# Kernel tuning notes

Hardware: AMD Instinct MI355X
Metric: run time of the kernel (lower is better)

The kernel has to match this reference:

```python
import jax, jax.numpy as jnp
import numpy as np

DIM = 1024
HEADS = 16
DIM_HEAD = 64
INNER = HEADS * DIM_HEAD  # 1024
MAX_POS = 512
B, N = 2, 1024


def setup_inputs() -> dict:
    key = jax.random.key(0)
    ks = jax.random.split(key, 6)
    s = DIM ** -0.5
    x = jax.random.normal(ks[0], (B, N, DIM), dtype=jnp.float32)
    Wq = jax.random.normal(ks[1], (DIM, INNER), dtype=jnp.float32) * s
    Wkv = jax.random.normal(ks[2], (DIM, 2 * INNER), dtype=jnp.float32) * s
    Wo = jax.random.normal(ks[3], (INNER, DIM), dtype=jnp.float32) * (INNER ** -0.5)
    bo = jnp.zeros((DIM,), dtype=jnp.float32)
    rel_emb = jax.random.normal(ks[4], (2 * MAX_POS + 1, DIM_HEAD), dtype=jnp.float32)
    return {"x": x, "Wq": Wq, "Wkv": Wkv, "Wo": Wo, "bo": bo, "rel_emb": rel_emb}


def reference(x, Wq, Wkv, Wo, bo, rel_emb):
    b, n, _ = x.shape
    scale = DIM_HEAD ** -0.5
    q = x @ Wq                    # [b, n, inner]
    kv = x @ Wkv                  # [b, n, 2*inner]
    k, v = jnp.split(kv, 2, axis=-1)

    def split_heads(t):
        return t.reshape(b, n, HEADS, DIM_HEAD).transpose(0, 2, 1, 3)  # [b,h,n,d]

    q, k, v = map(split_heads, (q, k, v))
    dots = jnp.einsum('bhid,bhjd->bhij', q, k) * scale

    seq = jnp.arange(n)
    dist = jnp.clip(seq[:, None] - seq[None, :], -MAX_POS, MAX_POS) + MAX_POS  # [n, n]
    rel = rel_emb[dist]           # [n, n, d]
    pos_attn = jnp.einsum('bhnd,nrd->bhnr', q, rel) * scale
    dots = dots + pos_attn

    attn = jax.nn.softmax(dots, axis=-1)
    out = jnp.einsum('bhij,bhjd->bhid', attn, v)
    out = out.transpose(0, 2, 1, 3).reshape(b, n, INNER)
    return out @ Wo + bo
```

## Files before the change

### kernel.cpp

```cpp
#include <hip/hip_runtime.h>

typedef __bf16 bf16x8 __attribute__((ext_vector_type(8)));
typedef float f32x4 __attribute__((ext_vector_type(4)));

#define DEV __device__ __forceinline__

DEV unsigned short f2bf(float f) {
  union { float f; unsigned u; } x; x.f = f;
  unsigned r = x.u + 0x7FFFu + ((x.u >> 16) & 1u);
  return (unsigned short)(r >> 16);
}
DEV float bf2f(unsigned short h) {
  union { unsigned u; float f; } x; x.u = ((unsigned)h) << 16;
  return x.f;
}
DEV unsigned short bfc(float f) {
  union { __bf16 b; unsigned short u; } c; c.b = (__bf16)f; return c.u;
}

typedef __attribute__((address_space(3))) void* lds_vp;
typedef const __attribute__((address_space(1))) void* gbl_vp;
DEV void load_lds16(const unsigned short* gp, void* lp) {
  __builtin_amdgcn_global_load_lds((gbl_vp)(const void*)gp, (lds_vp)lp, 16, 0, 0);
}

__global__ __launch_bounds__(256)
void prep_k(const float* __restrict__ x, const float* __restrict__ rel,
            const float* __restrict__ bo, const float* __restrict__ Wq,
            const float* __restrict__ Wkv, const float* __restrict__ Wo,
            unsigned short* __restrict__ xb, unsigned short* __restrict__ relb,
            unsigned short* __restrict__ bob, unsigned short* __restrict__ WqkvT,
            unsigned short* __restrict__ WoT) {
  __shared__ unsigned short tile[32][33];
  const int bid = blockIdx.x, tid = threadIdx.x;
  if (bid < 2114) {
    const float* src; unsigned short* dst; long base; long n;
    if (bid < 2048)      { src = x;   dst = xb;   base = (long)bid * 1024;          n = 2097152; }
    else if (bid < 2113) { src = rel; dst = relb; base = (long)(bid - 2048) * 1024; n = 65600; }
    else                 { src = bo;  dst = bob;  base = 0;                          n = 1024; }
    long i = base + tid * 4;
    if (i < n) {
      float4 v = *(const float4*)&src[i];
      unsigned long long u = (unsigned long long)f2bf(v.x)
                           | ((unsigned long long)f2bf(v.y) << 16)
                           | ((unsigned long long)f2bf(v.z) << 32)
                           | ((unsigned long long)f2bf(v.w) << 48);
      *(unsigned long long*)&dst[i] = u;
    }
  } else {
    int id = bid - 2114;
    const float* src; unsigned short* dst; const int R = 1024; int C, txt, tyt;
    if (id < 1024)      { src = Wq;  dst = WqkvT;           C = 1024; txt = id & 31; tyt = id >> 5; }
    else if (id < 3072) { int l = id - 1024; src = Wkv; dst = WqkvT + 1048576; C = 2048; txt = l & 63; tyt = l >> 6; }
    else                { int l = id - 3072; src = Wo;  dst = WoT;             C = 1024; txt = l & 31; tyt = l >> 5; }
    int c0 = txt * 32, r0 = tyt * 32;
    int tx = tid & 31, ty = tid >> 5;
    #pragma unroll
    for (int i = 0; i < 4; ++i)
      tile[ty + i * 8][tx] = f2bf(src[(size_t)(r0 + ty + i * 8) * C + c0 + tx]);
    __syncthreads();
    #pragma unroll
    for (int i = 0; i < 4; ++i)
      dst[(size_t)(c0 + ty + i * 8) * R + r0 + tx] = tile[tx][ty + i * 8];
  }
}

DEV void stage16(const unsigned short* gbase, size_t gstride,
                 unsigned short* lbase, int r0, int lane) {
  #pragma unroll
  for (int t = 0; t < 2; ++t) {
    int r = r0 + t * 8 + (lane >> 3);
    int lc = (lane & 7) ^ (r & 7);
    load_lds16(&gbase[(size_t)r * gstride + lc * 8], &lbase[(size_t)(r0 + t * 8) * 64]);
  }
}
DEV bf16x8 read_swz(const unsigned short* buf, int row, int lc) {
  int pc = lc ^ (row & 7);
  return *(const bf16x8*)&buf[row * 64 + pc * 8];
}

__global__ __launch_bounds__(256)
void gemm_qkv(const unsigned short* __restrict__ A,
              const unsigned short* __restrict__ Bt,
              unsigned short* __restrict__ o0,
              unsigned short* __restrict__ o1,
              unsigned short* __restrict__ o2) {
  __shared__ __align__(16) unsigned short As[64 * 64];
  __shared__ __align__(16) unsigned short Bs[128 * 64];
  __shared__ unsigned short tbuf[64][68];
  const int tid  = threadIdx.x;
  const int lane = tid & 63, wave = tid >> 6;
  const int q15  = lane & 15, quad = lane >> 4;
  const int wr = wave >> 1, wc = wave & 1;
  const int m0 = blockIdx.y * 64, n0 = blockIdx.x * 128;
  const int K = 1024;

  f32x4 acc[2][4] = {};
  for (int k0 = 0; k0 < K; k0 += 64) {
    __syncthreads();
    stage16(&A[(size_t)m0 * K + k0], K, As, wave * 16, lane);
    stage16(&Bt[(size_t)n0 * K + k0], K, Bs, wave * 32, lane);
    stage16(&Bt[(size_t)n0 * K + k0], K, Bs, wave * 32 + 16, lane);
    __syncthreads();
    #pragma unroll
    for (int ks = 0; ks < 2; ++ks) {
      bf16x8 af[2], bfr[4];
      #pragma unroll
      for (int i = 0; i < 2; ++i)
        af[i] = read_swz(As, wr * 32 + i * 16 + q15, ks * 4 + quad);
      #pragma unroll
      for (int j = 0; j < 4; ++j)
        bfr[j] = read_swz(Bs, wc * 64 + j * 16 + q15, ks * 4 + quad);
      #pragma unroll
      for (int i = 0; i < 2; ++i)
        #pragma unroll
        for (int j = 0; j < 4; ++j)
          acc[i][j] = __builtin_amdgcn_mfma_f32_16x16x32_bf16(af[i], bfr[j], acc[i][j], 0, 0, 0);
    }
  }

  const int b = m0 >> 10, nn0 = m0 & 1023;
  if (n0 < 2048) {
    #pragma unroll
    for (int i = 0; i < 2; ++i)
      #pragma unroll
      for (int j = 0; j < 4; ++j)
        #pragma unroll
        for (int r = 0; r < 4; ++r) {
          int row = m0 + wr * 32 + i * 16 + quad * 4 + r;
          int col = n0 + wc * 64 + j * 16 + q15;
          float v = acc[i][j][r];
          int nn = row & 1023;
          unsigned short* dst; int c = col; float sc = 1.f;
          if (col < 1024) { dst = o0; sc = 0.125f; }
          else            { dst = o1; c = col - 1024; }
          int h = c >> 6, dd = c & 63;
          dst[((size_t)((row >> 10) * 16 + h) * 1024 + nn) * 64 + dd] = f2bf(v * sc);
        }
  } else {
    const int hp = (n0 - 2048) >> 6;
    #pragma unroll
    for (int hh = 0; hh < 2; ++hh) {
      __syncthreads();
      if (wc == hh) {
        #pragma unroll
        for (int i = 0; i < 2; ++i)
          #pragma unroll
          for (int j = 0; j < 4; ++j)
            #pragma unroll
            for (int r = 0; r < 4; ++r)
              tbuf[wr * 32 + i * 16 + quad * 4 + r][j * 16 + q15] = f2bf(acc[i][j][r]);
      }
      __syncthreads();
      const int bh = b * 16 + hp + hh;
      const int d = tid >> 2, nb = (tid & 3) * 16;
      #pragma unroll
      for (int s = 0; s < 2; ++s) {
        int n = nb + s * 8;
        union { uint4 v; unsigned short us[8]; } t;
        #pragma unroll
        for (int e = 0; e < 8; ++e) t.us[e] = tbuf[n + e][d];
        *(uint4*)&o2[((size_t)bh * 64 + d) * 1024 + nn0 + n] = t.v;
      }
    }
  }
}

__global__ __launch_bounds__(512)
void flash_attn(const unsigned short* __restrict__ q_ws,
                const unsigned short* __restrict__ k_ws,
                const unsigned short* __restrict__ vt_ws,
                const unsigned short* __restrict__ rel,
                unsigned short* __restrict__ ao) {
  __shared__ __align__(16) unsigned short Kbuf[2][64 * 64];
  __shared__ __align__(16) unsigned short Vbuf[2][64 * 64];
  __shared__ __align__(16) unsigned short P_lds[8][16 * 64];
  union TXu {
    unsigned short T[8][16][84];
    float x[4][64][21];
  };
  __shared__ __align__(16) TXu tx;

  const int tid  = threadIdx.x;
  const int lane = tid & 63, w = tid >> 6;
  const int q15  = lane & 15, quad = lane >> 4;
  const int wr4  = w & 3, jh = w >> 2;
  const int bh = blockIdx.x;
  const int ib = blockIdx.y * 64 + wr4 * 16;

  const unsigned short* qp = q_ws  + (size_t)bh * 1024 * 64;
  const unsigned short* kp = k_ws  + (size_t)bh * 1024 * 64;
  const unsigned short* tp = vt_ws + (size_t)bh * 64 * 1024;

  unsigned short* Kb = &Kbuf[jh][0];
  unsigned short* Vb = &Vbuf[jh][0];

  bf16x8 aq[2];
  #pragma unroll
  for (int ks = 0; ks < 2; ++ks)
    aq[ks] = *(const bf16x8*)&qp[(size_t)(ib + q15) * 64 + ks * 32 + quad * 8];

  f32x4 o[4] = {};
  float l_i[4] = {0.f, 0.f, 0.f, 0.f};

  for (int jt = 0; jt < 8; ++jt) {
    const int j0 = jh * 512 + jt * 64;
    __syncthreads();
    stage16(kp + (size_t)j0 * 64, 64, Kb, wr4 * 16, lane);
    stage16(tp + j0, 1024, Vb, wr4 * 16, lane);

    int tb = ib - j0 + 512 - 63;
    f32x4 accT[5] = {};
    #pragma unroll
    for (int ks = 0; ks < 2; ++ks)
      #pragma unroll
      for (int ub = 0; ub < 5; ++ub) {
        int trow = tb + ub * 16 + q15;
        trow = trow < 0 ? 0 : (trow > 1024 ? 1024 : trow);
        bf16x8 br = *(const bf16x8*)&rel[(size_t)trow * 64 + ks * 32 + quad * 8];
        accT[ub] = __builtin_amdgcn_mfma_f32_16x16x32_bf16(aq[ks], br, accT[ub], 0, 0, 0);
      }
    #pragma unroll
    for (int ub = 0; ub < 5; ++ub)
      #pragma unroll
      for (int r = 0; r < 4; ++r)
        tx.T[w][quad * 4 + r][ub * 16 + q15] = bfc(accT[ub][r]);

    __syncthreads();

    f32x4 accS[4] = {};
    #pragma unroll
    for (int ks = 0; ks < 2; ++ks)
      #pragma unroll
      for (int cb = 0; cb < 4; ++cb) {
        bf16x8 bk = read_swz(Kb, cb * 16 + q15, ks * 4 + quad);
        accS[cb] = __builtin_amdgcn_mfma_f32_16x16x32_bf16(aq[ks], bk, accS[cb], 0, 0, 0);
      }

    #pragma unroll
    for (int r = 0; r < 4; ++r) {
      const int dl = quad * 4 + r;
      #pragma unroll
      for (int cb = 0; cb < 4; ++cb) {
        int dj = cb * 16 + q15;
        float s = accS[cb][r] + bf2f(tx.T[w][dl][63 + dl - dj]);
        float p = exp2f(fmaf(s, 1.44269504f, -64.f));
        l_i[r] += p;
        P_lds[w][dl * 64 + ((((dj >> 3) ^ (dl & 7)) << 3) | (dj & 7))] = bfc(p);
      }
    }

    #pragma unroll
    for (int ks = 0; ks < 2; ++ks) {
      bf16x8 ap = *(const bf16x8*)&P_lds[w][q15 * 64 + (((ks * 4 + quad) ^ (q15 & 7)) << 3)];
      #pragma unroll
      for (int db = 0; db < 4; ++db) {
        bf16x8 bv = read_swz(Vb, db * 16 + q15, ks * 4 + quad);
        o[db] = __builtin_amdgcn_mfma_f32_16x16x32_bf16(ap, bv, o[db], 0, 0, 0);
      }
    }
  }

  #pragma unroll
  for (int r = 0; r < 4; ++r)
    #pragma unroll
    for (int off = 1; off < 16; off <<= 1)
      l_i[r] += __shfl_xor(l_i[r], off, 64);

  __syncthreads();

  if (w >= 4) {
    float* xr = tx.x[w - 4][lane];
    #pragma unroll
    for (int db = 0; db < 4; ++db)
      #pragma unroll
      for (int r = 0; r < 4; ++r)
        xr[db * 4 + r] = o[db][r];
    #pragma unroll
    for (int r = 0; r < 4; ++r) xr[16 + r] = l_i[r];
  }
  __syncthreads();
  if (w < 4) {
    const float* xr = tx.x[w][lane];
    float inv[4];
    #pragma unroll
    for (int r = 0; r < 4; ++r)
      inv[r] = 1.f / (l_i[r] + xr[16 + r] + 1e-30f);
    const int b = bh >> 4, h = bh & 15;
    #pragma unroll
    for (int db = 0; db < 4; ++db)
      #pragma unroll
      for (int r = 0; r < 4; ++r) {
        int row = ib + quad * 4 + r;
        ao[((size_t)(b * 1024 + row)) * 1024 + h * 64 + db * 16 + q15] =
            bfc((o[db][r] + xr[db * 4 + r]) * inv[r]);
      }
  }
}

__global__ __launch_bounds__(256)
void gemm_out(const unsigned short* __restrict__ A,
              const unsigned short* __restrict__ Bt,
              const unsigned short* __restrict__ bias,
              float* __restrict__ fo) {
  __shared__ __align__(16) unsigned short As[64 * 64];
  __shared__ __align__(16) unsigned short Bs[64 * 64];
  const int tid  = threadIdx.x;
  const int lane = tid & 63, w = tid >> 6;
  const int q15  = lane & 15, quad = lane >> 4;
  const int m0 = blockIdx.y * 64, n0 = blockIdx.x * 64;
  const int K = 1024, N = 1024;

  f32x4 acc[4] = {};
  for (int k0 = 0; k0 < K; k0 += 64) {
    __syncthreads();
    stage16(&A[(size_t)m0 * K + k0], K, As, w * 16, lane);
    stage16(&Bt[(size_t)n0 * K + k0], K, Bs, w * 16, lane);
    __syncthreads();
    #pragma unroll
    for (int ks = 0; ks < 2; ++ks) {
      bf16x8 af = read_swz(As, w * 16 + q15, ks * 4 + quad);
      bf16x8 bfr[4];
      #pragma unroll
      for (int j = 0; j < 4; ++j)
        bfr[j] = read_swz(Bs, j * 16 + q15, ks * 4 + quad);
      #pragma unroll
      for (int j = 0; j < 4; ++j)
        acc[j] = __builtin_amdgcn_mfma_f32_16x16x32_bf16(af, bfr[j], acc[j], 0, 0, 0);
    }
  }
  #pragma unroll
  for (int j = 0; j < 4; ++j)
    #pragma unroll
    for (int r = 0; r < 4; ++r) {
      int row = m0 + w * 16 + quad * 4 + r;
      int col = n0 + j * 16 + q15;
      fo[(size_t)row * N + col] = acc[j][r] + bf2f(bias[col]);
    }
}

extern "C" void kernel_launch(void* const* d_in, const int* in_sizes, int n_in,
                              void* d_out, int out_size, void* d_ws, size_t ws_size,
                              hipStream_t stream) {
  (void)in_sizes; (void)n_in; (void)out_size; (void)ws_size;
  const float* x   = (const float*)d_in[0];
  const float* Wq  = (const float*)d_in[1];
  const float* Wkv = (const float*)d_in[2];
  const float* Wo  = (const float*)d_in[3];
  const float* bo  = (const float*)d_in[4];
  const float* rel = (const float*)d_in[5];
  float* out = (float*)d_out;

  unsigned short* ws = (unsigned short*)d_ws;
  unsigned short* WoT   = ws;
  unsigned short* relb  = WoT   + 1048576;
  unsigned short* bob   = relb  + 65664;
  unsigned short* q_ws  = bob   + 1088;
  unsigned short* k_ws  = q_ws  + 2097152;
  unsigned short* vT    = k_ws  + 2097152;
  unsigned short* WqkvT = vT    + 2097152;
  unsigned short* xb    = WqkvT + 3145728;
  unsigned short* ao    = WqkvT;

  prep_k<<<6210, 256, 0, stream>>>(x, rel, bo, Wq, Wkv, Wo,
                                   xb, relb, bob, WqkvT, WoT);
  gemm_qkv<<<dim3(24, 32), 256, 0, stream>>>(xb, WqkvT, q_ws, k_ws, vT);
  flash_attn<<<dim3(32, 16), 512, 0, stream>>>(q_ws, k_ws, vT, relb, ao);
  gemm_out<<<dim3(16, 32), 256, 0, stream>>>(ao, WoT, bob, out);
}
```

Baseline: 157.5 us.

## Swap MFMA operand order to transpose accumulators and vectorize LDS/global stores

Swaps the A/B operands of every MFMA in the attention kernel so each lane holds four consecutive key or dim columns of one query row instead of four rows. That lets the rel-bias tile, the P tile and the final output be written as packed 64-bit LDS stores, and shrinks the row-sum reduction to two cross-quad shuffles. The output is staged through LDS and written to global memory as 16-byte vector stores instead of scattered 2-byte stores. The cost is extra LDS traffic and a repurposed K buffer in the epilogue, with some risk of new bank conflicts.

```diff
diff --git a/kernel.cpp b/kernel.cpp
--- a/kernel.cpp
+++ b/kernel.cpp
@@ -177,7 +177,7 @@
   __shared__ __align__(16) unsigned short P_lds[8][16 * 64];
   union TXu {
     unsigned short T[8][16][84];
-    float x[4][64][21];
+    float bnc[4][65][17];
   };
   __shared__ __align__(16) TXu tx;
 
@@ -194,6 +194,8 @@
 
   unsigned short* Kb = &Kbuf[jh][0];
   unsigned short* Vb = &Vbuf[jh][0];
+  unsigned short* Trow = &tx.T[w][q15][0];
+  unsigned short* Prow = &P_lds[w][q15 * 64];
 
   bf16x8 aq[2];
   #pragma unroll
@@ -201,7 +203,7 @@
     aq[ks] = *(const bf16x8*)&qp[(size_t)(ib + q15) * 64 + ks * 32 + quad * 8];
 
   f32x4 o[4] = {};
-  float l_i[4] = {0.f, 0.f, 0.f, 0.f};
+  float l_acc = 0.f;
 
   for (int jt = 0; jt < 8; ++jt) {
     const int j0 = jh * 512 + jt * 64;
@@ -218,13 +220,15 @@
         int trow = tb + ub * 16 + q15;
         trow = trow < 0 ? 0 : (trow > 1024 ? 1024 : trow);
         bf16x8 br = *(const bf16x8*)&rel[(size_t)trow * 64 + ks * 32 + quad * 8];
-        accT[ub] = __builtin_amdgcn_mfma_f32_16x16x32_bf16(aq[ks], br, accT[ub], 0, 0, 0);
-      }
-    #pragma unroll
-    for (int ub = 0; ub < 5; ++ub)
-      #pragma unroll
-      for (int r = 0; r < 4; ++r)
-        tx.T[w][quad * 4 + r][ub * 16 + q15] = bfc(accT[ub][r]);
+        accT[ub] = __builtin_amdgcn_mfma_f32_16x16x32_bf16(br, aq[ks], accT[ub], 0, 0, 0);
+      }
+    #pragma unroll
+    for (int ub = 0; ub < 5; ++ub) {
+      uint2 tw;
+      tw.x = (unsigned)bfc(accT[ub][0]) | ((unsigned)bfc(accT[ub][1]) << 16);
+      tw.y = (unsigned)bfc(accT[ub][2]) | ((unsigned)bfc(accT[ub][3]) << 16);
+      *(uint2*)&Trow[ub * 16 + quad * 4] = tw;
+    }
 
     __syncthreads();
 
@@ -234,67 +238,75 @@
       #pragma unroll
       for (int cb = 0; cb < 4; ++cb) {
         bf16x8 bk = read_swz(Kb, cb * 16 + q15, ks * 4 + quad);
-        accS[cb] = __builtin_amdgcn_mfma_f32_16x16x32_bf16(aq[ks], bk, accS[cb], 0, 0, 0);
-      }
-
-    #pragma unroll
-    for (int r = 0; r < 4; ++r) {
-      const int dl = quad * 4 + r;
-      #pragma unroll
-      for (int cb = 0; cb < 4; ++cb) {
-        int dj = cb * 16 + q15;
-        float s = accS[cb][r] + bf2f(tx.T[w][dl][63 + dl - dj]);
-        float p = exp2f(fmaf(s, 1.44269504f, -64.f));
-        l_i[r] += p;
-        P_lds[w][dl * 64 + ((((dj >> 3) ^ (dl & 7)) << 3) | (dj & 7))] = bfc(p);
-      }
+        accS[cb] = __builtin_amdgcn_mfma_f32_16x16x32_bf16(bk, aq[ks], accS[cb], 0, 0, 0);
+      }
+
+    #pragma unroll
+    for (int cb = 0; cb < 4; ++cb) {
+      float p[4];
+      #pragma unroll
+      for (int r = 0; r < 4; ++r) {
+        int jl = cb * 16 + quad * 4 + r;
+        float s = accS[cb][r] + bf2f(Trow[63 + q15 - jl]);
+        p[r] = exp2f(fmaf(s, 1.44269504f, -64.f));
+        l_acc += p[r];
+      }
+      uint2 pw;
+      pw.x = (unsigned)bfc(p[0]) | ((unsigned)bfc(p[1]) << 16);
+      pw.y = (unsigned)bfc(p[2]) | ((unsigned)bfc(p[3]) << 16);
+      int phys = (cb * 2 + (quad >> 1)) ^ (q15 & 7);
+      *(uint2*)&Prow[phys * 8 + (quad & 1) * 4] = pw;
     }
 
     #pragma unroll
     for (int ks = 0; ks < 2; ++ks) {
-      bf16x8 ap = *(const bf16x8*)&P_lds[w][q15 * 64 + (((ks * 4 + quad) ^ (q15 & 7)) << 3)];
+      bf16x8 ap = *(const bf16x8*)&Prow[(((ks * 4 + quad) ^ (q15 & 7))) * 8];
       #pragma unroll
       for (int db = 0; db < 4; ++db) {
         bf16x8 bv = read_swz(Vb, db * 16 + q15, ks * 4 + quad);
-        o[db] = __builtin_amdgcn_mfma_f32_16x16x32_bf16(ap, bv, o[db], 0, 0, 0);
-      }
-    }
-  }
-
-  #pragma unroll
-  for (int r = 0; r < 4; ++r)
-    #pragma unroll
-    for (int off = 1; off < 16; off <<= 1)
-      l_i[r] += __shfl_xor(l_i[r], off, 64);
+        o[db] = __builtin_amdgcn_mfma_f32_16x16x32_bf16(bv, ap, o[db], 0, 0, 0);
+      }
+    }
+  }
+
+  l_acc += __shfl_xor(l_acc, 16, 64);
+  l_acc += __shfl_xor(l_acc, 32, 64);
 
   __syncthreads();
 
   if (w >= 4) {
-    float* xr = tx.x[w - 4][lane];
+    const int ww = w - 4;
     #pragma unroll
     for (int db = 0; db < 4; ++db)
       #pragma unroll
       for (int r = 0; r < 4; ++r)
-        xr[db * 4 + r] = o[db][r];
-    #pragma unroll
-    for (int r = 0; r < 4; ++r) xr[16 + r] = l_i[r];
+        tx.bnc[ww][db * 16 + quad * 4 + r][q15] = o[db][r];
+    tx.bnc[ww][64][q15] = l_acc;
   }
   __syncthreads();
   if (w < 4) {
-    const float* xr = tx.x[w][lane];
-    float inv[4];
-    #pragma unroll
-    for (int r = 0; r < 4; ++r)
-      inv[r] = 1.f / (l_i[r] + xr[16 + r] + 1e-30f);
+    float lB = tx.bnc[w][64][q15];
+    float inv = 1.f / (l_acc + lB + 1e-30f);
+    unsigned short* Bt = (unsigned short*)&Kbuf[0][0] + (size_t)w * 16 * 72;
+    #pragma unroll
+    for (int db = 0; db < 4; ++db) {
+      float v0 = (o[db][0] + tx.bnc[w][db * 16 + quad * 4 + 0][q15]) * inv;
+      float v1 = (o[db][1] + tx.bnc[w][db * 16 + quad * 4 + 1][q15]) * inv;
+      float v2 = (o[db][2] + tx.bnc[w][db * 16 + quad * 4 + 2][q15]) * inv;
+      float v3 = (o[db][3] + tx.bnc[w][db * 16 + quad * 4 + 3][q15]) * inv;
+      uint2 bw;
+      bw.x = (unsigned)bfc(v0) | ((unsigned)bfc(v1) << 16);
+      bw.y = (unsigned)bfc(v2) | ((unsigned)bfc(v3) << 16);
+      *(uint2*)&Bt[q15 * 72 + db * 16 + quad * 4] = bw;
+    }
+    const int il = lane >> 2, ch = (lane & 3) * 16;
+    bf16x8 u0 = *(const bf16x8*)&Bt[il * 72 + ch];
+    bf16x8 u1 = *(const bf16x8*)&Bt[il * 72 + ch + 8];
     const int b = bh >> 4, h = bh & 15;
-    #pragma unroll
-    for (int db = 0; db < 4; ++db)
-      #pragma unroll
-      for (int r = 0; r < 4; ++r) {
-        int row = ib + quad * 4 + r;
-        ao[((size_t)(b * 1024 + row)) * 1024 + h * 64 + db * 16 + q15] =
-            bfc((o[db][r] + xr[db * 4 + r]) * inv[r]);
-      }
+    size_t addr = ((size_t)(b * 1024 + blockIdx.y * 64 + w * 16 + il)) * 1024
+                + h * 64 + ch;
+    *(bf16x8*)&ao[addr] = u0;
+    *(bf16x8*)&ao[addr + 8] = u1;
   }
 }
 
```

After: 157.8 us. Within noise of the previous version (+0.2%).
